# Kernel tuning notes

Measured on AMD Instinct MI355X. Metric: run time of the kernel, lower is better.

The kernel has to match this reference:

```python
import jax, jax.numpy as jnp
import numpy as np

B, H, W_IMG, C = 256, 88, 88, 3
NUM_CH = 64
MATCH_ATOL = 0.0


def setup_inputs() -> dict:
    key = jax.random.key(0)
    k1, k2 = jax.random.split(key)
    rgb = jax.random.randint(k1, (B, H, W_IMG, C), 0, 256, dtype=jnp.int32)
    # conv params: HWIO layout for lax.conv_general_dilated
    Wc = jax.random.normal(k2, (8, 8, C, NUM_CH), dtype=jnp.float32) * 0.05
    bc = jnp.zeros((NUM_CH,), dtype=jnp.float32)
    return {"rgb": rgb, "Wc": Wc, "bc": bc}


def _guidance_from_feats(out):
    # out: [B, 121, 64]
    # pairwise feature-equality counts (O(N^2) broadcast, as in original)
    eq = jnp.max(jnp.abs(out[:, None, :, :] - out[:, :, None, :]), axis=-1) <= MATCH_ATOL
    counts = jnp.sum(eq, axis=-1)  # [B, 121] int32, always >= 1 (self-match)
    M = counts.shape[-1]
    hist = jax.vmap(lambda c: jnp.bincount(c, length=M + 1))(counts)  # [B, M+1]
    cum = jnp.cumsum(hist, axis=-1)
    K = int(0.3 * M)
    allow_freq = cum <= K
    kmin = jnp.min(counts, axis=-1)  # [B]
    allow_freq = jnp.logical_or(allow_freq, jnp.arange(M + 1)[None, :] == kmin[:, None])
    # gather allow flag per position via its count value
    mask_keep = jnp.take_along_axis(allow_freq[:, None, :], counts[..., None], axis=-1)[..., 0]
    fcounts = counts.astype(jnp.float32)
    logits = jnp.where(mask_keep, -jnp.log(fcounts), -jnp.inf)
    attn = jax.nn.softmax(logits, axis=-1)  # [B, 121]
    guidance = attn.reshape(attn.shape[0], 1, 11, 11)
    return jax.lax.stop_gradient(guidance)


def reference(rgb, Wc, bc):
    x = rgb.astype(jnp.float32) / 255.0  # [B, 88, 88, 3]
    feats = jax.lax.conv_general_dilated(
        x, Wc, window_strides=(8, 8), padding='VALID',
        dimension_numbers=('NHWC', 'HWIO', 'NHWC')) + bc
    feats = jax.nn.relu(feats)  # [B, 11, 11, 64]
    vis_op = feats.reshape(feats.shape[0], -1, feats.shape[-1])  # [B, 121, 64]
    guidance = _guidance_from_feats(vis_op)  # [B, 1, 11, 11]
    return (vis_op, guidance)
```

## Files before the change

### kernel.cpp

```cpp
#include <hip/hip_runtime.h>
#include <hip/hip_bf16.h>

#define B_SZ 256
#define NCH 64
#define NPOS 121
#define NPATCH (B_SZ * NPOS)
#define KTOT 192
#define RGB_W 264
#define LDR 264
#define FST 68

typedef short bf16x8 __attribute__((ext_vector_type(8)));
typedef float f32x4 __attribute__((ext_vector_type(4)));

static __device__ inline unsigned f2bf(float x) {
  union { float f; unsigned u; } a; a.f = x;
  return (a.u + 0x7FFFu + ((a.u >> 16) & 1u)) >> 16;
}
static __device__ inline unsigned pack2(float lo, float hi) {
  return f2bf(lo) | (f2bf(hi) << 16);
}

__global__ __launch_bounds__(256) void pack_b(const float* __restrict__ Wc,
                                              unsigned short* __restrict__ Btg) {
  const int n = threadIdx.x & 63;
  const int q = threadIdx.x >> 6;
  const int k0 = q * 48;
  float w[48];
  #pragma unroll
  for (int j = 0; j < 48; ++j) w[j] = Wc[(k0 + j) * NCH + n];
  #pragma unroll
  for (int c = 0; c < 6; ++c) {
    uint4 p;
    p.x = pack2(w[c*8+0], w[c*8+1]); p.y = pack2(w[c*8+2], w[c*8+3]);
    p.z = pack2(w[c*8+4], w[c*8+5]); p.w = pack2(w[c*8+6], w[c*8+7]);
    *(uint4*)&Btg[n * KTOT + k0 + c * 8] = p;
  }
}

__global__ __launch_bounds__(256) void fused(
    const int* __restrict__ rgb, const unsigned short* __restrict__ Btg,
    const float* __restrict__ bc, float* __restrict__ out,
    float* __restrict__ gout) {
  __shared__ __align__(16) unsigned short rgbL[88 * LDR];
  __shared__ unsigned sig[NPOS];
  __shared__ int counts[NPOS];
  __shared__ int redi[4];
  __shared__ float redf[4];
  unsigned* fbits = (unsigned*)rgbL;

  const int b = blockIdx.x, tid = threadIdx.x;
  const int lane = tid & 63, w = tid >> 6;
  const int lr = lane & 15, lg = lane >> 4;

  bf16x8 bfr[4][6];
  #pragma unroll
  for (int ni = 0; ni < 4; ++ni)
    #pragma unroll
    for (int ks = 0; ks < 6; ++ks)
      bfr[ni][ks] = *(const bf16x8*)&Btg[(ni * 16 + lr) * KTOT + ks * 32 + lg * 8];

  const int4* src4 = (const int4*)(rgb + (size_t)b * 88 * RGB_W);
  #pragma unroll 4
  for (int it = 0; it < 22; ++it) {
    const int i = tid + it * 256;
    const int4 t = src4[i];
    const int e = i * 4, row = e / RGB_W, col = e - row * RGB_W;
    uint2 p;
    p.x = pack2((float)t.x * (1.f/255.f), (float)t.y * (1.f/255.f));
    p.y = pack2((float)t.z * (1.f/255.f), (float)t.w * (1.f/255.f));
    *(uint2*)&rgbL[row * LDR + col] = p;
  }
  {
    const int i = tid + 5632;
    if (i < 5808) {
      const int4 t = src4[i];
      const int e = i * 4, row = e / RGB_W, col = e - row * RGB_W;
      uint2 p;
      p.x = pack2((float)t.x * (1.f/255.f), (float)t.y * (1.f/255.f));
      p.y = pack2((float)t.z * (1.f/255.f), (float)t.w * (1.f/255.f));
      *(uint2*)&rgbL[row * LDR + col] = p;
    }
  }
  __syncthreads();

  const int m0 = w * 32;
  f32x4 acc[2][4] = {};
  int kyv[6], kmv[6];
  #pragma unroll
  for (int ks = 0; ks < 6; ++ks) {
    const int k0 = ks * 32 + lg * 8;
    kyv[ks] = k0 / 24; kmv[ks] = k0 - kyv[ks] * 24;
  }
  #pragma unroll
  for (int mi = 0; mi < 2; ++mi) {
    const int p = m0 + mi * 16 + lr;
    const int pe = p > 120 ? 120 : p;
    const int oy = pe / 11, ox = pe - oy * 11;
    #pragma unroll
    for (int ks = 0; ks < 6; ++ks) {
      const bf16x8 a =
          *(const bf16x8*)&rgbL[(oy * 8 + kyv[ks]) * LDR + ox * 24 + kmv[ks]];
      #pragma unroll
      for (int ni = 0; ni < 4; ++ni)
        acc[mi][ni] = __builtin_amdgcn_mfma_f32_16x16x32_bf16(
            a, bfr[ni][ks], acc[mi][ni], 0, 0, 0);
    }
  }
  __syncthreads();

  float bias[4];
  #pragma unroll
  for (int ni = 0; ni < 4; ++ni) bias[ni] = bc[ni * 16 + lr];
  float* outB = out + (size_t)b * NPOS * NCH;
  #pragma unroll
  for (int mi = 0; mi < 2; ++mi) {
    #pragma unroll
    for (int rr = 0; rr < 4; ++rr) {
      const int p = m0 + mi * 16 + lg * 4 + rr;
      if (p < NPOS) {
        #pragma unroll
        for (int ni = 0; ni < 4; ++ni) {
          const int col = ni * 16 + lr;
          const float v = fmaxf(acc[mi][ni][rr] + bias[ni], 0.f) + 0.f;
          outB[p * NCH + col] = v;
          fbits[p * FST + col] = __float_as_uint(v);
        }
      }
    }
  }
  __syncthreads();

  if (tid < NPOS) {
    const uint4* fr = (const uint4*)&fbits[tid * FST];
    unsigned h = 0;
    #pragma unroll
    for (int q = 0; q < 16; ++q) {
      const uint4 v = fr[q];
      h ^= (v.x ^ (v.x >> 15)) * ((8u*q + 1u) * 0x9E3779B9u);
      h ^= (v.y ^ (v.y >> 15)) * ((8u*q + 3u) * 0x9E3779B9u);
      h ^= (v.z ^ (v.z >> 15)) * ((8u*q + 5u) * 0x9E3779B9u);
      h ^= (v.w ^ (v.w >> 15)) * ((8u*q + 7u) * 0x9E3779B9u);
    }
    sig[tid] = h;
  }
  __syncthreads();

  int cnt = 0x7fffffff;
  if (tid < NPOS) {
    const unsigned si = sig[tid];
    int m = 0;
    for (int j = 0; j < NPOS; ++j) m += (sig[j] == si) ? 1 : 0;
    cnt = 1;
    if (m > 1) {
      cnt = 0;
      for (int j = 0; j < NPOS; ++j) {
        if (sig[j] == si) {
          int eq = 1;
          for (int c = 0; c < NCH; ++c) eq &= (fbits[tid*FST + c] == fbits[j*FST + c]);
          cnt += eq;
        }
      }
    }
    counts[tid] = cnt;
  }
  __syncthreads();

  int km_ = cnt;
  #pragma unroll
  for (int off = 1; off < 64; off <<= 1) km_ = min(km_, __shfl_xor(km_, off, 64));
  if (lane == 0) redi[w] = km_;
  __syncthreads();
  const int kmin = min(min(redi[0], redi[1]), min(redi[2], redi[3]));

  float wv = 0.f;
  if (tid < NPOS) {
    int cum = 0;
    for (int j = 0; j < NPOS; ++j) cum += (counts[j] <= cnt) ? 1 : 0;
    if (cum <= 36 || cnt == kmin) wv = 1.f / (float)cnt;
  }
  float s = wv;
  #pragma unroll
  for (int off = 1; off < 64; off <<= 1) s += __shfl_xor(s, off, 64);
  if (lane == 0) redf[w] = s;
  __syncthreads();
  const float Z = redf[0] + redf[1] + redf[2] + redf[3];
  if (tid < NPOS) gout[(size_t)b * NPOS + tid] = wv / Z;
}

extern "C" void kernel_launch(void* const* d_in, const int* in_sizes, int n_in,
                              void* d_out, int out_size, void* d_ws, size_t ws_size,
                              hipStream_t stream) {
  const int*   rgb = (const int*)d_in[0];
  const float* Wc  = (const float*)d_in[1];
  const float* bc  = (const float*)d_in[2];
  float* out   = (float*)d_out;
  float* guide = out + (size_t)NPATCH * NCH;
  unsigned short* Btg = (unsigned short*)d_ws;

  pack_b<<<1, 256, 0, stream>>>(Wc, Btg);
  fused<<<B_SZ, 256, 0, stream>>>(rgb, Btg, bc, out, guide);
}
```

Measured before the change: 84.17 us.

## Fold weight packing into fused kernel, use 512 threads and batch loads

Removes the separate pack_b launch: each block now converts the fp32 conv weights to bf16 into shared memory itself. The block grows to 512 threads (8 waves, one 16-row M tile each instead of two per wave). All RGB int4 loads are issued up front into registers before any conversion, so more memory requests are in flight. This saves a kernel launch and the dependency between launches, at the cost of redundant per-block weight conversion, more LDS use and more register pressure.

```diff
diff --git a/kernel.cpp b/kernel.cpp
--- a/kernel.cpp
+++ b/kernel.cpp
@@ -8,6 +8,7 @@
 #define KTOT 192
 #define RGB_W 264
 #define LDR 264
+#define LDB 200
 #define FST 68
 
 typedef short bf16x8 __attribute__((ext_vector_type(8)));
@@ -21,90 +22,71 @@
   return f2bf(lo) | (f2bf(hi) << 16);
 }
 
-__global__ __launch_bounds__(256) void pack_b(const float* __restrict__ Wc,
-                                              unsigned short* __restrict__ Btg) {
-  const int n = threadIdx.x & 63;
-  const int q = threadIdx.x >> 6;
-  const int k0 = q * 48;
-  float w[48];
-  #pragma unroll
-  for (int j = 0; j < 48; ++j) w[j] = Wc[(k0 + j) * NCH + n];
-  #pragma unroll
-  for (int c = 0; c < 6; ++c) {
-    uint4 p;
-    p.x = pack2(w[c*8+0], w[c*8+1]); p.y = pack2(w[c*8+2], w[c*8+3]);
-    p.z = pack2(w[c*8+4], w[c*8+5]); p.w = pack2(w[c*8+6], w[c*8+7]);
-    *(uint4*)&Btg[n * KTOT + k0 + c * 8] = p;
-  }
-}
-
-__global__ __launch_bounds__(256) void fused(
-    const int* __restrict__ rgb, const unsigned short* __restrict__ Btg,
+__global__ __launch_bounds__(512) void fused(
+    const int* __restrict__ rgb, const float* __restrict__ Wc,
     const float* __restrict__ bc, float* __restrict__ out,
     float* __restrict__ gout) {
   __shared__ __align__(16) unsigned short rgbL[88 * LDR];
+  __shared__ __align__(16) unsigned short BtL[NCH * LDB];
   __shared__ unsigned sig[NPOS];
   __shared__ int counts[NPOS];
-  __shared__ int redi[4];
-  __shared__ float redf[4];
+  __shared__ int redi[8];
+  __shared__ float redf[8];
   unsigned* fbits = (unsigned*)rgbL;
 
   const int b = blockIdx.x, tid = threadIdx.x;
   const int lane = tid & 63, w = tid >> 6;
   const int lr = lane & 15, lg = lane >> 4;
 
-  bf16x8 bfr[4][6];
-  #pragma unroll
-  for (int ni = 0; ni < 4; ++ni)
+  {
     #pragma unroll
-    for (int ks = 0; ks < 6; ++ks)
-      bfr[ni][ks] = *(const bf16x8*)&Btg[(ni * 16 + lr) * KTOT + ks * 32 + lg * 8];
+    for (int j = 0; j < 12; ++j) {
+      const int k = w * 24 + 2 * j;
+      const float w0 = Wc[k * NCH + lane];
+      const float w1 = Wc[(k + 1) * NCH + lane];
+      *(unsigned*)&BtL[lane * LDB + k] = pack2(w0, w1);
+    }
+  }
 
   const int4* src4 = (const int4*)(rgb + (size_t)b * 88 * RGB_W);
-  #pragma unroll 4
-  for (int it = 0; it < 22; ++it) {
-    const int i = tid + it * 256;
-    const int4 t = src4[i];
+  int4 r[11];
+  #pragma unroll
+  for (int it = 0; it < 11; ++it) r[it] = src4[tid + it * 512];
+  int4 rt;
+  const bool tail = (tid < 176);
+  if (tail) rt = src4[5632 + tid];
+  #pragma unroll
+  for (int it = 0; it < 11; ++it) {
+    const int i = tid + it * 512;
     const int e = i * 4, row = e / RGB_W, col = e - row * RGB_W;
     uint2 p;
-    p.x = pack2((float)t.x * (1.f/255.f), (float)t.y * (1.f/255.f));
-    p.y = pack2((float)t.z * (1.f/255.f), (float)t.w * (1.f/255.f));
+    p.x = pack2((float)r[it].x * (1.f/255.f), (float)r[it].y * (1.f/255.f));
+    p.y = pack2((float)r[it].z * (1.f/255.f), (float)r[it].w * (1.f/255.f));
     *(uint2*)&rgbL[row * LDR + col] = p;
   }
-  {
-    const int i = tid + 5632;
-    if (i < 5808) {
-      const int4 t = src4[i];
-      const int e = i * 4, row = e / RGB_W, col = e - row * RGB_W;
-      uint2 p;
-      p.x = pack2((float)t.x * (1.f/255.f), (float)t.y * (1.f/255.f));
-      p.y = pack2((float)t.z * (1.f/255.f), (float)t.w * (1.f/255.f));
-      *(uint2*)&rgbL[row * LDR + col] = p;
-    }
+  if (tail) {
+    const int i = 5632 + tid;
+    const int e = i * 4, row = e / RGB_W, col = e - row * RGB_W;
+    uint2 p;
+    p.x = pack2((float)rt.x * (1.f/255.f), (float)rt.y * (1.f/255.f));
+    p.y = pack2((float)rt.z * (1.f/255.f), (float)rt.w * (1.f/255.f));
+    *(uint2*)&rgbL[row * LDR + col] = p;
   }
   __syncthreads();
 
-  const int m0 = w * 32;
-  f32x4 acc[2][4] = {};
-  int kyv[6], kmv[6];
+  const int p = w * 16 + lr;
+  const int pe = p > 120 ? 120 : p;
+  const int oy = pe / 11, ox = pe - oy * 11;
+  f32x4 acc[4] = {};
   #pragma unroll
   for (int ks = 0; ks < 6; ++ks) {
     const int k0 = ks * 32 + lg * 8;
-    kyv[ks] = k0 / 24; kmv[ks] = k0 - kyv[ks] * 24;
-  }
-  #pragma unroll
-  for (int mi = 0; mi < 2; ++mi) {
-    const int p = m0 + mi * 16 + lr;
-    const int pe = p > 120 ? 120 : p;
-    const int oy = pe / 11, ox = pe - oy * 11;
+    const int ky = k0 / 24, km = k0 - ky * 24;
+    const bf16x8 a = *(const bf16x8*)&rgbL[(oy * 8 + ky) * LDR + ox * 24 + km];
     #pragma unroll
-    for (int ks = 0; ks < 6; ++ks) {
-      const bf16x8 a =
-          *(const bf16x8*)&rgbL[(oy * 8 + kyv[ks]) * LDR + ox * 24 + kmv[ks]];
-      #pragma unroll
-      for (int ni = 0; ni < 4; ++ni)
-        acc[mi][ni] = __builtin_amdgcn_mfma_f32_16x16x32_bf16(
-            a, bfr[ni][ks], acc[mi][ni], 0, 0, 0);
+    for (int ni = 0; ni < 4; ++ni) {
+      const bf16x8 bb = *(const bf16x8*)&BtL[(ni * 16 + lr) * LDB + k0];
+      acc[ni] = __builtin_amdgcn_mfma_f32_16x16x32_bf16(a, bb, acc[ni], 0, 0, 0);
     }
   }
   __syncthreads();
@@ -114,18 +96,14 @@
   for (int ni = 0; ni < 4; ++ni) bias[ni] = bc[ni * 16 + lr];
   float* outB = out + (size_t)b * NPOS * NCH;
   #pragma unroll
-  for (int mi = 0; mi < 2; ++mi) {
-    #pragma unroll
-    for (int rr = 0; rr < 4; ++rr) {
-      const int p = m0 + mi * 16 + lg * 4 + rr;
-      if (p < NPOS) {
-        #pragma unroll
-        for (int ni = 0; ni < 4; ++ni) {
-          const int col = ni * 16 + lr;
-          const float v = fmaxf(acc[mi][ni][rr] + bias[ni], 0.f) + 0.f;
-          outB[p * NCH + col] = v;
-          fbits[p * FST + col] = __float_as_uint(v);
-        }
+  for (int rr = 0; rr < 4; ++rr) {
+    const int ps = w * 16 + lg * 4 + rr;
+    if (ps < NPOS) {
+      #pragma unroll
+      for (int ni = 0; ni < 4; ++ni) {
+        const float v = fmaxf(acc[ni][rr] + bias[ni], 0.f) + 0.f;
+        outB[ps * NCH + ni * 16 + lr] = v;
+        fbits[ps * FST + ni * 16 + lr] = __float_as_uint(v);
       }
     }
   }
@@ -171,7 +149,9 @@
   for (int off = 1; off < 64; off <<= 1) km_ = min(km_, __shfl_xor(km_, off, 64));
   if (lane == 0) redi[w] = km_;
   __syncthreads();
-  const int kmin = min(min(redi[0], redi[1]), min(redi[2], redi[3]));
+  int kmin = redi[0];
+  #pragma unroll
+  for (int q = 1; q < 8; ++q) kmin = min(kmin, redi[q]);
 
   float wv = 0.f;
   if (tid < NPOS) {
@@ -184,7 +164,9 @@
   for (int off = 1; off < 64; off <<= 1) s += __shfl_xor(s, off, 64);
   if (lane == 0) redf[w] = s;
   __syncthreads();
-  const float Z = redf[0] + redf[1] + redf[2] + redf[3];
+  float Z = redf[0];
+  #pragma unroll
+  for (int q = 1; q < 8; ++q) Z += redf[q];
   if (tid < NPOS) gout[(size_t)b * NPOS + tid] = wv / Z;
 }
 
@@ -196,8 +178,6 @@
   const float* bc  = (const float*)d_in[2];
   float* out   = (float*)d_out;
   float* guide = out + (size_t)NPATCH * NCH;
-  unsigned short* Btg = (unsigned short*)d_ws;
 
-  pack_b<<<1, 256, 0, stream>>>(Wc, Btg);
-  fused<<<B_SZ, 256, 0, stream>>>(rgb, Btg, bc, out, guide);
+  fused<<<B_SZ, 512, 0, stream>>>(rgb, Wc, bc, out, guide);
 }
```

New measurement: 77.79 us (median of 2 runs). 1.08x faster.
